# Optimization experiments

Measured on AMD Instinct MI355X. Metric: run time of the kernel, lower is better.

## Reference

```python
import jax, jax.numpy as jnp
import numpy as np

NH = 4       # n_heads
R = 3        # n_rounds
LN_EPS = 1e-5
NEG = -1e9   # large negative for masked attention (avoids NaN on fully-masked rows)


def _mha(q, k, v, w, b, block=None):
    # w: [4, D, D] = (Wq, Wk, Wv, Wo); b: [4, D]. batch_first MHA, no dropout (eval).
    B, Nq, Dm = q.shape
    hd = Dm // NH

    def proj(x, wi, bi):
        return (x @ wi + bi).reshape(B, -1, NH, hd).transpose(0, 2, 1, 3)  # [B,h,N,hd]

    Q = proj(q, w[0], b[0])
    K = proj(k, w[1], b[1])
    V = proj(v, w[2], b[2])
    s = jnp.einsum('bhqd,bhkd->bhqk', Q, K) * (1.0 / np.sqrt(hd))
    if block is not None:  # block[b,q,k]=True means masked out
        s = jnp.where(block[:, None, :, :], NEG, s)
    p = jax.nn.softmax(s, axis=-1)
    o = jnp.einsum('bhqk,bhkd->bhqd', p, V).transpose(0, 2, 1, 3).reshape(B, -1, Dm)
    return o @ w[3] + b[3]


def setup_inputs() -> dict:
    key = jax.random.key(0)
    ks = jax.random.split(key, 16)
    B, N, Dm = 256, 128, 256
    s = 0.02
    return {
        'H': jax.random.normal(ks[0], (B, N, Dm), jnp.float32),
        'pred_heads': jax.random.randint(ks[1], (B, N), 0, N),
        'mask': jnp.ones((B, N), jnp.float32),
        'ha_w': jax.random.normal(ks[2], (R, 4, Dm, Dm)) * s,
        'ha_b': jnp.zeros((R, 4, Dm)),
        'sa_w': jax.random.normal(ks[3], (R, 4, Dm, Dm)) * s,
        'sa_b': jnp.zeros((R, 4, Dm)),
        'ct_w': jax.random.normal(ks[4], (R, 2 * Dm, Dm)) * s,
        'ct_b': jnp.zeros((R, Dm)),
        'gate_w': jax.random.normal(ks[5], (R, 4 * Dm, Dm)) * s,
        'gate_b': jnp.zeros((R, Dm)),
        'tr_w': jax.random.normal(ks[6], (R, 4 * Dm, Dm)) * s,
        'tr_b': jnp.zeros((R, Dm)),
        'ln_g': jnp.ones((R, Dm)),
        'ln_b': jnp.zeros((R, Dm)),
        'arc_head_w': jax.random.normal(ks[7], (Dm, Dm)) * s,
        'arc_head_b': jnp.zeros((Dm,)),
        'arc_dep_w': jax.random.normal(ks[8], (Dm, Dm)) * s,
        'arc_dep_b': jnp.zeros((Dm,)),
        'bilinear': jax.random.normal(ks[9], (Dm, Dm)) * np.sqrt(2.0 / Dm).astype(np.float32),
        'bh_w': jax.random.normal(ks[10], (Dm,)) * s,
        'bh_b': jnp.zeros(()),
        'bd_w': jax.random.normal(ks[11], (Dm,)) * s,
        'bd_b': jnp.zeros(()),
    }


def reference(H, pred_heads, mask, ha_w, ha_b, sa_w, sa_b, ct_w, ct_b,
              gate_w, gate_b, tr_w, tr_b, ln_g, ln_b,
              arc_head_w, arc_head_b, arc_dep_w, arc_dep_b, bilinear,
              bh_w, bh_b, bd_w, bd_b):
    B, N, Dm = H.shape
    mb = mask > 0
    hi = jnp.clip(pred_heads, 0, N - 1)
    hi3 = jnp.broadcast_to(hi[:, :, None], (B, N, Dm))
    bidx = jnp.arange(B)[:, None]
    eye = jnp.eye(N, dtype=bool)
    # sibling mask: same predicted head, not self, both positions valid (constant across rounds)
    sib = (pred_heads[:, :, None] == pred_heads[:, None, :]) & ~eye[None] \
          & mb[:, None, :] & mb[:, :, None]
    block = ~sib

    Hr = H
    for i in range(R):
        # gather head representation, attend to it
        head_repr = jnp.take_along_axis(Hr, hi3, axis=1)
        head_msg = _mha(Hr, head_repr, head_repr, ha_w[i], ha_b[i])
        # scatter-add children onto their heads, average
        child_sum = jnp.zeros_like(Hr).at[bidx, hi].add(Hr)
        child_count = jnp.zeros((B, N), Hr.dtype).at[bidx, hi].add(mask)
        child_avg = child_sum / jnp.maximum(child_count, 1.0)[:, :, None]
        child_msg = jax.nn.gelu(
            jnp.concatenate([Hr, child_avg], -1) @ ct_w[i] + ct_b[i], approximate=False)
        # masked sibling self-attention (N <= 128 branch)
        sib_msg = _mha(Hr, Hr, Hr, sa_w[i], sa_b[i], block=block)
        # gated fuse + residual + LayerNorm
        comb = jnp.concatenate([Hr, head_msg, child_msg, sib_msg], -1)
        g = jax.nn.sigmoid(comb @ gate_w[i] + gate_b[i])
        u = jax.nn.gelu(comb @ tr_w[i] + tr_b[i], approximate=False)
        Hn = Hr + g * u
        mu = Hn.mean(-1, keepdims=True)
        var = ((Hn - mu) ** 2).mean(-1, keepdims=True)
        Hr = (Hn - mu) / jnp.sqrt(var + LN_EPS) * ln_g[i] + ln_b[i]

    h_head = Hr @ arc_head_w + arc_head_b
    h_dep = Hr @ arc_dep_w + arc_dep_b
    scores = jnp.einsum('bnd,de,bme->bnm', h_head, bilinear, h_dep)
    scores = scores + (h_head @ bh_w + bh_b)[:, None, :] + (h_dep @ bd_w + bd_b)[:, :, None]
    return Hr, scores
```

## Files before the change

### kernel.cpp

```cpp
#include <hip/hip_runtime.h>
#include <hip/hip_bf16.h>
#include <math.h>

typedef __hip_bfloat16 bf16;
typedef __attribute__((ext_vector_type(8))) short bf16x8v;
typedef __attribute__((ext_vector_type(4))) float f32x4v;

#define BD 256
#define NN 128
#define DM 256
#define NHD 4
#define HDIM 64
#define RR 3

__device__ __forceinline__ float b2f(bf16 x) { return __bfloat162float(x); }
__device__ __forceinline__ bf16 f2b(float x) { return __float2bfloat16(x); }
__device__ __forceinline__ float geluf(float x) { return 0.5f * x * (1.f + erff(x * 0.70710678118654752f)); }

#define GLOAD16(g, l) __builtin_amdgcn_global_load_lds( \
    (const __attribute__((address_space(1))) void*)(g), \
    (__attribute__((address_space(3))) void*)(l), 16, 0, 0)

__global__ __launch_bounds__(256) void cvt32to16_kernel(
    const float* __restrict__ in, bf16* __restrict__ out, int n)
{
  int i = blockIdx.x * 256 + threadIdx.x;
  int stride = gridDim.x * 256;
  for (; i < n; i += stride) out[i] = f2b(in[i]);
}

__global__ __launch_bounds__(256) void cvt16to32_kernel(
    const bf16* __restrict__ in, float* __restrict__ out, int n)
{
  int i = blockIdx.x * 256 + threadIdx.x;
  int stride = gridDim.x * 256;
  for (; i < n; i += stride) out[i] = b2f(in[i]);
}

struct TDesc { const float* src; bf16* dst; int K; int base; };
struct TTable { TDesc e[12]; };

__global__ __launch_bounds__(256) void transpose_w_kernel(TTable T, int nent)
{
  int t = blockIdx.x;
  int ei = 0;
  for (int i = 1; i < nent; i++) if (t >= T.e[i].base) ei = i;
  const float* src = T.e[ei].src;
  bf16* dst = T.e[ei].dst;
  int K = T.e[ei].K;
  int lt = t - T.e[ei].base;
  int nt = lt & 7, kt = lt >> 3;

  __shared__ float tile[32][33];
  int tx = threadIdx.x & 31, ty = threadIdx.x >> 5;
#pragma unroll
  for (int i = 0; i < 4; i++)
    tile[ty + i * 8][tx] = src[(size_t)(kt * 32 + ty + i * 8) * 256 + nt * 32 + tx];
  __syncthreads();
#pragma unroll
  for (int i = 0; i < 4; i++)
    dst[(size_t)(nt * 32 + ty + i * 8) * K + kt * 32 + tx] = f2b(tile[tx][ty + i * 8]);
}

struct FJob { const float* A; const float* B; bf16* outT; int koff; int kst; };
struct FJobs { FJob j[13]; };

__global__ __launch_bounds__(256) void wfuse_kernel(FJobs F)
{
  const FJob jb = F.j[blockIdx.y];
  const int k0 = blockIdx.x * 16;
  const int col = threadIdx.x;
  float acc[16];
#pragma unroll
  for (int i = 0; i < 16; i++) acc[i] = 0.f;
  for (int m = 0; m < 256; m++) {
    float bv = jb.B[(size_t)m * 256 + col];
#pragma unroll
    for (int i = 0; i < 16; i++)
      acc[i] += jb.A[(size_t)(k0 + i) * 256 + m] * bv;
  }
#pragma unroll
  for (int i = 0; i < 16; i++)
    jb.outT[(size_t)col * jb.kst + jb.koff + k0 + i] = f2b(acc[i]);
}

__global__ __launch_bounds__(256) void bfuse_kernel(
    const float* gate_w, const float* tr_w, const float* gate_b, const float* tr_b,
    const float* ha_b, const float* sa_b,
    const float* ahw, const float* ahb, const float* bil,
    const float* bhw, const float* bhb,
    float* fgb, float* ftb, float* fab_bias, float* vha, float* cha)
{
  int blk = blockIdx.x, col = threadIdx.x;
  if (blk < 6) {
    int r = blk >> 1; bool isT = blk & 1;
    const float* W  = (isT ? tr_w : gate_w) + (size_t)r * 262144;
    const float* b0 = (isT ? tr_b : gate_b) + (size_t)r * 256;
    const float* boh = ha_b + (size_t)r * 1024 + 768;
    const float* bos = sa_b + (size_t)r * 1024 + 768;
    float acc = b0[col];
    for (int m = 0; m < 256; m++) {
      acc += boh[m] * W[(size_t)(256 + m) * 256 + col];
      acc += bos[m] * W[(size_t)(768 + m) * 256 + col];
    }
    ((isT ? ftb : fgb) + (size_t)r * 256)[col] = acc;
  } else {
    float a1 = 0.f, a2 = 0.f;
    for (int m = 0; m < 256; m++) {
      a1 += ahb[m] * bil[(size_t)m * 256 + col];
      a2 += ahw[(size_t)col * 256 + m] * bhw[m];
    }
    fab_bias[col] = a1;
    vha[col] = a2;
    if (col == 0) {
      float c = bhb[0];
      for (int m = 0; m < 256; m++) c += ahb[m] * bhw[m];
      cha[0] = c;
    }
  }
}

struct ProjArgs {
  const bf16* Hc; const bf16* CA; const int* gather;
  const bf16* W[7];
  const float* bias[7];
  bf16* out[7];
};

__global__ __launch_bounds__(256) void proj_fused_kernel(ProjArgs P)
{
  const int b  = blockIdx.x & 255;
  const int nh = blockIdx.x >> 8;
  const int c0 = nh * 128;
  const int tid = threadIdx.x;
  const int w = tid >> 6;
  const int lane = tid & 63;
  const int wr = w >> 1, wc = w & 1;
  const int r16 = lane & 15;
  const int kg = lane >> 4;

  __shared__ __align__(16) char lds[81920];

  const char* Hb = (const char*)(P.Hc + (size_t)b * NN * DM);

#pragma unroll
  for (int i = 0; i < 16; i++) {
    int row = w * 32 + i * 2 + (lane >> 5);
    int src = row * 512 + (((lane & 31) * 16) ^ ((row & 7) << 4));
    GLOAD16(Hb + src, lds + w * 16384 + i * 1024);
  }

#define STAGE_W(WT, K2, KT, BUF) do { \
    _Pragma("unroll") \
    for (int i_ = 0; i_ < 2; i_++) { \
      int wrow_ = w * 32 + i_ * 16 + (lane >> 2); \
      int slot_ = (lane & 3) ^ ((wrow_ >> 1) & 3); \
      GLOAD16((const char*)(WT) + (size_t)(c0 + wrow_) * (K2) + (KT) * 64 + slot_ * 16, \
              lds + 65536 + (BUF) * 8192 + w * 2048 + i_ * 1024); \
    } } while (0)

  STAGE_W(P.W[0], 512, 0, 0);
  __syncthreads();

  int lrow[4], grow[4];
#pragma unroll
  for (int mi = 0; mi < 4; mi++) {
    lrow[mi] = wr * 64 + mi * 16 + r16;
    int g = P.gather[b * NN + lrow[mi]];
    grow[mi] = min(max(g, 0), NN - 1);
  }
  int wro[4];
#pragma unroll
  for (int ni = 0; ni < 4; ni++) {
    int ct_ = wc * 64 + ni * 16 + r16;
    wro[ni] = ct_ * 64 + ((kg ^ ((ct_ >> 1) & 3)) << 4);
  }

  const bf16* CAb = P.CA + (size_t)b * NN * DM;
  int buf = 0;
  f32x4v zero = {0.f, 0.f, 0.f, 0.f};

#pragma unroll
  for (int j = 0; j < 7; j++) {
    const bool GATH = (j == 1) || (j == 2);
    const bool TR   = (j == 2) || (j == 5);
    const bool ACT  = (j == 6);
    const int NKS = (j == 6) ? 16 : 8;
    const int K2  = (j == 6) ? 1024 : 512;
    const bf16* Wj  = P.W[j];
    const bf16* Wj1 = (j < 6) ? P.W[j + 1] : P.W[j];
    const int  K2n  = (j < 6) ? ((j + 1 == 6) ? 1024 : 512) : K2;

    f32x4v acc[4][4];
#pragma unroll
    for (int mi = 0; mi < 4; mi++)
#pragma unroll
      for (int ni = 0; ni < 4; ni++) acc[mi][ni] = zero;

    for (int kt = 0; kt < NKS; kt++) {
      if (!(j == 6 && kt + 1 == NKS)) {
        const bf16* Wn = (kt + 1 < NKS) ? Wj : Wj1;
        int nkt = (kt + 1 < NKS) ? kt + 1 : 0;
        int nK2 = (kt + 1 < NKS) ? K2 : K2n;
        STAGE_W(Wn, nK2, nkt, buf ^ 1);
      }

      bf16x8v a[4], wv[4];
      if (j == 6 && kt >= 8) {
#pragma unroll
        for (int mi = 0; mi < 4; mi++)
          a[mi] = *(const bf16x8v*)(CAb + (size_t)lrow[mi] * DM + (kt - 8) * 32 + kg * 8);
      } else {
#pragma unroll
        for (int mi = 0; mi < 4; mi++) {
          int ar = GATH ? grow[mi] : lrow[mi];
          int off = ar * 512 + (((kt * 64) + kg * 16) ^ ((ar & 7) << 4));
          a[mi] = *(const bf16x8v*)(lds + off);
        }
      }
#pragma unroll
      for (int ni = 0; ni < 4; ni++)
        wv[ni] = *(const bf16x8v*)(lds + 65536 + buf * 8192 + wro[ni]);

#pragma unroll
      for (int mi = 0; mi < 4; mi++)
#pragma unroll
        for (int ni = 0; ni < 4; ni++)
          acc[mi][ni] = __builtin_amdgcn_mfma_f32_16x16x32_bf16(a[mi], wv[ni], acc[mi][ni], 0, 0, 0);

      __syncthreads();
      buf ^= 1;
    }

    bf16* outj = P.out[j];
    const float* bj = P.bias[j];
#pragma unroll
    for (int ni = 0; ni < 4; ni++) {
      int col = c0 + wc * 64 + ni * 16 + r16;
      float bv = bj ? bj[col] : 0.f;
#pragma unroll
      for (int mi = 0; mi < 4; mi++) {
        int row0 = wr * 64 + mi * 16 + kg * 4;
        if (!TR) {
          size_t base = ((size_t)b * NN + row0) * DM + col;
#pragma unroll
          for (int r = 0; r < 4; r++) {
            float x = acc[mi][ni][r] + bv;
            if (ACT) x = geluf(x);
            outj[base + (size_t)r * DM] = f2b(x);
          }
        } else {
          size_t base = ((size_t)b * DM + col) * NN + row0;
#pragma unroll
          for (int r = 0; r < 4; r++)
            outj[base + r] = f2b(acc[mi][ni][r] + bv);
        }
      }
    }
  }
#undef STAGE_W
}

struct GJob {
  const bf16 *a0, *a1, *a2, *a3;
  const int* gather;
  const bf16* Wt;
  const float* bias;
  bf16* out;
  int K, act, transp;
};
struct GJobs8 { GJob j[8]; };

__global__ __launch_bounds__(256) void gemm_multi_kernel(GJobs8 J)
{
  const GJob jb = J.j[blockIdx.y];
  const int b  = blockIdx.x & 255;
  const int nh = blockIdx.x >> 8;
  const int tid = threadIdx.x;
  const int w = tid >> 6;
  const int lane = tid & 63;
  const int wr = w >> 1, wc = w & 1;
  const int r16 = lane & 15;
  const int kg = lane >> 4;
  const int K = jb.K;
  const int nk = K >> 5;
  const int c0 = nh * 128;

  __shared__ __align__(16) char lds[32768];

  const int srow = tid >> 2;
  const int skc  = tid & 3;
  const int sl   = skc ^ ((srow >> 1) & 3);
  int g0 = srow, g1 = srow + 64;
  if (jb.gather) {
    int t0 = jb.gather[b * NN + srow];      g0 = min(max(t0, 0), NN - 1);
    int t1 = jb.gather[b * NN + srow + 64]; g1 = min(max(t1, 0), NN - 1);
  }
  const size_t aoff0 = ((size_t)b * NN + g0) * DM + sl * 8;
  const size_t aoff1 = ((size_t)b * NN + g1) * DM + sl * 8;
  const bf16* wsrc0 = jb.Wt + (size_t)(c0 + srow) * K + sl * 8;
  const bf16* wsrc1 = jb.Wt + (size_t)(c0 + srow + 64) * K + sl * 8;
  const int wbase = w * 1024;

  f32x4v zero = {0.f, 0.f, 0.f, 0.f};
  f32x4v acc[4][4];
#pragma unroll
  for (int mi = 0; mi < 4; mi++)
#pragma unroll
    for (int ni = 0; ni < 4; ni++) acc[mi][ni] = zero;

  int a_ro[4], w_ro[4];
#pragma unroll
  for (int mi = 0; mi < 4; mi++) {
    int row = wr * 64 + mi * 16 + r16;
    a_ro[mi] = row * 64 + ((kg ^ ((row >> 1) & 3)) << 4);
  }
#pragma unroll
  for (int ni = 0; ni < 4; ni++) {
    int col = wc * 64 + ni * 16 + r16;
    w_ro[ni] = col * 64 + ((kg ^ ((col >> 1) & 3)) << 4);
  }

  {
    const bf16* Ab = jb.a0;
    GLOAD16(Ab + aoff0, lds + wbase);
    GLOAD16(Ab + aoff1, lds + 4096 + wbase);
    GLOAD16(wsrc0,      lds + 16384 + wbase);
    GLOAD16(wsrc1,      lds + 16384 + 4096 + wbase);
  }
  __syncthreads();

  int cur = 0;
  for (int kt = 0; kt < nk; kt++) {
    if (kt + 1 < nk) {
      int k0 = (kt + 1) << 5;
      int sg = k0 >> 8;
      const bf16* Ab = (sg == 0) ? jb.a0 : ((sg == 1) ? jb.a1 : ((sg == 2) ? jb.a2 : jb.a3));
      int ko = k0 & 255;
      int nb = (cur ^ 1) * 8192;
      GLOAD16(Ab + aoff0 + ko,  lds + nb + wbase);
      GLOAD16(Ab + aoff1 + ko,  lds + nb + 4096 + wbase);
      GLOAD16(wsrc0 + k0,       lds + 16384 + nb + wbase);
      GLOAD16(wsrc1 + k0,       lds + 16384 + nb + 4096 + wbase);
    }

    const char* La = lds + cur * 8192;
    const char* Lw = lds + 16384 + cur * 8192;
    bf16x8v a[4], ww[4];
#pragma unroll
    for (int mi = 0; mi < 4; mi++) a[mi] = *(const bf16x8v*)(La + a_ro[mi]);
#pragma unroll
    for (int ni = 0; ni < 4; ni++) ww[ni] = *(const bf16x8v*)(Lw + w_ro[ni]);
#pragma unroll
    for (int mi = 0; mi < 4; mi++)
#pragma unroll
      for (int ni = 0; ni < 4; ni++)
        acc[mi][ni] = __builtin_amdgcn_mfma_f32_16x16x32_bf16(a[mi], ww[ni], acc[mi][ni], 0, 0, 0);

    __syncthreads();
    cur ^= 1;
  }

#pragma unroll
  for (int ni = 0; ni < 4; ni++) {
    int col = c0 + wc * 64 + ni * 16 + r16;
    float bv = jb.bias ? jb.bias[col] : 0.f;
#pragma unroll
    for (int mi = 0; mi < 4; mi++) {
      int row0 = wr * 64 + mi * 16 + kg * 4;
      if (!jb.transp) {
        size_t base = ((size_t)b * NN + row0) * DM + col;
#pragma unroll
        for (int r = 0; r < 4; r++) {
          float x = acc[mi][ni][r] + bv;
          if (jb.act == 1) x = geluf(x);
          jb.out[base + (size_t)r * DM] = f2b(x);
        }
      } else {
        size_t base = ((size_t)b * DM + col) * NN + row0;
#pragma unroll
        for (int r = 0; r < 4; r++) {
          float x = acc[mi][ni][r] + bv;
          if (jb.act == 1) x = geluf(x);
          jb.out[base + r] = f2b(x);
        }
      }
    }
  }
}

struct AttnArgs {
  const bf16 *Qa, *Ka, *Va; bf16* Oa;
  const bf16 *Qs, *Ks, *Vs; bf16* Os;
};

__global__ __launch_bounds__(256) void attn2_kernel(
    AttnArgs A, const int* __restrict__ ph, const float* __restrict__ mask)
{
  const int b = blockIdx.y, h = blockIdx.x;
  const bool has_mask = (blockIdx.z == 1);
  const bf16* Qb = has_mask ? A.Qs : A.Qa;
  const bf16* Kb = has_mask ? A.Ks : A.Ka;
  const bf16* Vt = has_mask ? A.Vs : A.Va;
  bf16* Ob       = has_mask ? A.Os : A.Oa;

  const int w = threadIdx.x >> 6;
  const int lane = threadIdx.x & 63;
  const int r16 = lane & 15, kg = lane >> 4;
  const int q0 = w * 32;

  __shared__ bf16 P_lds[4][32 * 128];
  __shared__ int   ph_sh[NN];
  __shared__ float mk_sh[NN];

  if (has_mask && threadIdx.x < NN) {
    ph_sh[threadIdx.x] = ph[(size_t)b * NN + threadIdx.x];
    mk_sh[threadIdx.x] = mask[(size_t)b * NN + threadIdx.x];
  }
  __syncthreads();

  const bf16* Qh = Qb + (size_t)b * NN * DM + (size_t)h * HDIM;
  const bf16* Kh = Kb + (size_t)b * NN * DM + (size_t)h * HDIM;
  const bf16* Vh = Vt + ((size_t)b * DM + (size_t)h * HDIM) * NN;

  f32x4v zero = {0.f, 0.f, 0.f, 0.f};

  f32x4v accs[2][8];
#pragma unroll
  for (int mi = 0; mi < 2; mi++)
#pragma unroll
    for (int ni = 0; ni < 8; ni++) accs[mi][ni] = zero;

#pragma unroll
  for (int ks = 0; ks < 2; ks++) {
    int d = ks * 32 + kg * 8;
    bf16x8v a[2], bb[8];
#pragma unroll
    for (int mi = 0; mi < 2; mi++)
      a[mi] = *(const bf16x8v*)(Qh + (size_t)(q0 + mi * 16 + r16) * DM + d);
#pragma unroll
    for (int ni = 0; ni < 8; ni++)
      bb[ni] = *(const bf16x8v*)(Kh + (size_t)(ni * 16 + r16) * DM + d);
#pragma unroll
    for (int mi = 0; mi < 2; mi++)
#pragma unroll
      for (int ni = 0; ni < 8; ni++)
        accs[mi][ni] = __builtin_amdgcn_mfma_f32_16x16x32_bf16(a[mi], bb[ni], accs[mi][ni], 0, 0, 0);
  }

#pragma unroll
  for (int mi = 0; mi < 2; mi++) {
#pragma unroll
    for (int r = 0; r < 4; r++) {
      int wq = mi * 16 + kg * 4 + r;
      int q_e = q0 + wq;
      float v[8];
      float mx = -3.0e38f;
      int qp = 0; float qm = 1.f;
      if (has_mask) { qp = ph_sh[q_e]; qm = mk_sh[q_e]; }
#pragma unroll
      for (int ni = 0; ni < 8; ni++) {
        float s = accs[mi][ni][r] * 0.125f;
        if (has_mask) {
          int t_e = ni * 16 + r16;
          bool sib = (qp == ph_sh[t_e]) && (q_e != t_e) && (qm > 0.f) && (mk_sh[t_e] > 0.f);
          if (!sib) s = -1e9f;
        }
        v[ni] = s;
        mx = fmaxf(mx, s);
      }
#pragma unroll
      for (int o = 1; o < 16; o <<= 1) mx = fmaxf(mx, __shfl_xor(mx, o, 64));
      float sum = 0.f;
#pragma unroll
      for (int ni = 0; ni < 8; ni++) { v[ni] = __expf(v[ni] - mx); sum += v[ni]; }
#pragma unroll
      for (int o = 1; o < 16; o <<= 1) sum += __shfl_xor(sum, o, 64);
      float inv = 1.f / sum;
      int swz = (wq & 7) << 3;
#pragma unroll
      for (int ni = 0; ni < 8; ni++) {
        int t_e = ni * 16 + r16;
        P_lds[w][(wq * 128 + t_e) ^ swz] = f2b(v[ni] * inv);
      }
    }
  }
  __syncthreads();

  f32x4v acco[2][4];
#pragma unroll
  for (int mi = 0; mi < 2; mi++)
#pragma unroll
    for (int ni = 0; ni < 4; ni++) acco[mi][ni] = zero;

#pragma unroll
  for (int kt = 0; kt < 4; kt++) {
    int t = kt * 32 + kg * 8;
    bf16x8v a[2], bb[4];
#pragma unroll
    for (int mi = 0; mi < 2; mi++) {
      int wqr = mi * 16 + r16;
      int idx = (wqr * 128 + t) ^ ((wqr & 7) << 3);
      a[mi] = *(const bf16x8v*)&P_lds[w][idx];
    }
#pragma unroll
    for (int ni = 0; ni < 4; ni++)
      bb[ni] = *(const bf16x8v*)(Vh + (size_t)(ni * 16 + r16) * NN + t);
#pragma unroll
    for (int mi = 0; mi < 2; mi++)
#pragma unroll
      for (int ni = 0; ni < 4; ni++)
        acco[mi][ni] = __builtin_amdgcn_mfma_f32_16x16x32_bf16(a[mi], bb[ni], acco[mi][ni], 0, 0, 0);
  }

#pragma unroll
  for (int ni = 0; ni < 4; ni++) {
    int d = ni * 16 + r16;
#pragma unroll
    for (int mi = 0; mi < 2; mi++) {
      int qrow = q0 + mi * 16 + kg * 4;
      size_t base = ((size_t)b * NN + qrow) * DM + (size_t)h * HDIM + d;
#pragma unroll
      for (int r = 0; r < 4; r++)
        Ob[base + (size_t)r * DM] = f2b(acco[mi][ni][r]);
    }
  }
}

__global__ __launch_bounds__(256) void child_avg2_kernel(
    const bf16* __restrict__ Hr, const int* __restrict__ ph,
    const float* __restrict__ mask, bf16* __restrict__ CA)
{
  const int b = blockIdx.x;
  const int t = threadIdx.x;
  __shared__ int hi[NN];
  __shared__ float mk[NN];
  __shared__ int cnt[NN], off[NN], rnk[NN], lst[NN];
  __shared__ float cntf[NN];

  if (t < NN) {
    int g = ph[(size_t)b * NN + t];
    hi[t] = min(max(g, 0), NN - 1);
    mk[t] = mask[(size_t)b * NN + t];
  }
  __syncthreads();
  if (t < NN) {
    int c = 0, r = 0; float cf = 0.f;
    int me = hi[t];
    for (int j = 0; j < NN; j++) {
      int hj = hi[j];
      c  += (hj == t);
      cf += (hj == t) ? mk[j] : 0.f;
      r  += (j < t) && (hj == me);
    }
    cnt[t] = c; cntf[t] = cf; rnk[t] = r;
  }
  __syncthreads();
  if (t < NN) {
    int o = 0;
    for (int m = 0; m < t; m++) o += cnt[m];
    off[t] = o;
  }
  __syncthreads();
  if (t < NN) lst[off[hi[t]] + rnk[t]] = t;
  __syncthreads();

  const bf16* Hb = Hr + (size_t)b * NN * DM;
  bf16* Cb = CA + (size_t)b * NN * DM;
  const int d = t;
  for (int m = 0; m < NN; m++) {
    float s = 0.f;
    int o = off[m], c = cnt[m];
    for (int i = 0; i < c; i++)
      s += b2f(Hb[(size_t)lst[o + i] * DM + d]);
    Cb[(size_t)m * DM + d] = f2b(s / fmaxf(cntf[m], 1.f));
  }
}

__global__ __launch_bounds__(256) void ln_epi_kernel(
    const bf16* __restrict__ Hr, const bf16* __restrict__ Gp, const bf16* __restrict__ Up,
    const float* __restrict__ lg, const float* __restrict__ lb, bf16* __restrict__ Hout)
{
  const int b = blockIdx.y;
  const int m0 = blockIdx.x * 8;
  const int c = threadIdx.x;
  __shared__ float red[8];
  float lgv = lg[c], lbv = lb[c];
  int wv = c >> 6, ln = c & 63;
  for (int m = 0; m < 8; m++) {
    size_t idx = ((size_t)b * NN + m0 + m) * DM + c;
    float g = 1.f / (1.f + __expf(-b2f(Gp[idx])));
    float u = geluf(b2f(Up[idx]));
    float hn = b2f(Hr[idx]) + g * u;
    float s1 = hn, s2 = hn * hn;
#pragma unroll
    for (int o = 1; o < 64; o <<= 1) { s1 += __shfl_xor(s1, o, 64); s2 += __shfl_xor(s2, o, 64); }
    if (ln == 0) { red[wv] = s1; red[4 + wv] = s2; }
    __syncthreads();
    float sum = red[0] + red[1] + red[2] + red[3];
    float sq  = red[4] + red[5] + red[6] + red[7];
    float mu = sum * (1.f / DM);
    float var = sq * (1.f / DM) - mu * mu;
    float y = (hn - mu) * rsqrtf(var + 1e-5f) * lgv + lbv;
    Hout[idx] = f2b(y);
    __syncthreads();
  }
}

__global__ __launch_bounds__(256) void rhrd2_kernel(
    const bf16* __restrict__ Hc, const bf16* __restrict__ hd,
    const float* __restrict__ vha, const float* __restrict__ cha,
    const float* __restrict__ bdw, const float* __restrict__ bdb,
    float* __restrict__ rh, float* __restrict__ rd)
{
  int b = blockIdx.x;
  int t = threadIdx.x;
  int n = t & 127;
  bool isD = t >= 128;
  if (!isD) {
    const bf16* row = Hc + ((size_t)b * NN + n) * DM;
    float s = cha[0];
    for (int k = 0; k < DM; k++) s += b2f(row[k]) * vha[k];
    rh[(size_t)b * NN + n] = s;
  } else {
    const bf16* row = hd + ((size_t)b * NN + n) * DM;
    float s = bdb[0];
    for (int k = 0; k < DM; k++) s += b2f(row[k]) * bdw[k];
    rd[(size_t)b * NN + n] = s;
  }
}

__global__ __launch_bounds__(512) void scores_mfma_kernel(
    const bf16* __restrict__ tmp, const bf16* __restrict__ hd,
    const float* __restrict__ rh, const float* __restrict__ rd,
    float* __restrict__ out)
{
  const int b = blockIdx.x;
  const int w = threadIdx.x >> 6;
  const int lane = threadIdx.x & 63;
  const int wr = w >> 1, wc = w & 1;
  const int r16 = lane & 15;
  const int kg = lane >> 4;

  size_t qoff[2], moff[4];
#pragma unroll
  for (int mi = 0; mi < 2; mi++) qoff[mi] = ((size_t)b * NN + wr * 32 + mi * 16 + r16) * DM;
#pragma unroll
  for (int ni = 0; ni < 4; ni++) moff[ni] = ((size_t)b * NN + wc * 64 + ni * 16 + r16) * DM;

  f32x4v zero = {0.f, 0.f, 0.f, 0.f};
  f32x4v acc[2][4];
#pragma unroll
  for (int mi = 0; mi < 2; mi++)
#pragma unroll
    for (int ni = 0; ni < 4; ni++) acc[mi][ni] = zero;

  for (int k0 = 0; k0 < DM; k0 += 32) {
    int k = k0 + kg * 8;
    bf16x8v a[2], bb[4];
#pragma unroll
    for (int mi = 0; mi < 2; mi++) a[mi] = *(const bf16x8v*)(tmp + qoff[mi] + k);
#pragma unroll
    for (int ni = 0; ni < 4; ni++) bb[ni] = *(const bf16x8v*)(hd + moff[ni] + k);
#pragma unroll
    for (int mi = 0; mi < 2; mi++)
#pragma unroll
      for (int ni = 0; ni < 4; ni++)
        acc[mi][ni] = __builtin_amdgcn_mfma_f32_16x16x32_bf16(a[mi], bb[ni], acc[mi][ni], 0, 0, 0);
  }

#pragma unroll
  for (int ni = 0; ni < 4; ni++) {
    int m = wc * 64 + ni * 16 + r16;
    float rhm = rh[b * NN + m];
#pragma unroll
    for (int mi = 0; mi < 2; mi++) {
      int q0 = wr * 32 + mi * 16 + kg * 4;
#pragma unroll
      for (int r = 0; r < 4; r++)
        out[(size_t)b * NN * NN + (size_t)(q0 + r) * NN + m] =
            acc[mi][ni][r] + rhm + rd[b * NN + q0 + r];
    }
  }
}

extern "C" void kernel_launch(void* const* d_in, const int* in_sizes, int n_in,
                              void* d_out, int out_size, void* d_ws, size_t ws_size,
                              hipStream_t stream) {
  const float* H      = (const float*)d_in[0];
  const int*   ph     = (const int*)  d_in[1];
  const float* mask   = (const float*)d_in[2];
  const float* ha_w   = (const float*)d_in[3];
  const float* ha_b   = (const float*)d_in[4];
  const float* sa_w   = (const float*)d_in[5];
  const float* sa_b   = (const float*)d_in[6];
  const float* ct_w   = (const float*)d_in[7];
  const float* ct_b   = (const float*)d_in[8];
  const float* gate_w = (const float*)d_in[9];
  const float* gate_b = (const float*)d_in[10];
  const float* tr_w   = (const float*)d_in[11];
  const float* tr_b   = (const float*)d_in[12];
  const float* ln_g   = (const float*)d_in[13];
  const float* ln_b   = (const float*)d_in[14];
  const float* ahw    = (const float*)d_in[15];
  const float* ahb    = (const float*)d_in[16];
  const float* adw    = (const float*)d_in[17];
  const float* adb    = (const float*)d_in[18];
  const float* bil    = (const float*)d_in[19];
  const float* bhw    = (const float*)d_in[20];
  const float* bhb    = (const float*)d_in[21];
  const float* bdw    = (const float*)d_in[22];
  const float* bdb    = (const float*)d_in[23];

  const size_t AB = (size_t)BD * NN * DM;
  bf16* wsb  = (bf16*)d_ws;
  bf16* Hcur = wsb + 0 * AB;
  bf16* Qa   = wsb + 1 * AB;
  bf16* Ka   = wsb + 2 * AB;
  bf16* Va   = wsb + 3 * AB;
  bf16* Qs   = wsb + 4 * AB;
  bf16* Ks   = wsb + 5 * AB;
  bf16* Vs   = wsb + 6 * AB;
  bf16* mC   = wsb + 7 * AB;
  float* rh  = (float*)(wsb + 8 * AB);
  float* rd  = rh + (size_t)BD * NN;
  float* fgb = rd + (size_t)BD * NN;
  float* ftb = fgb + 768;
  float* fab_bias = ftb + 768;
  float* vha = fab_bias + 256;
  float* cha = vha + 256;

  bf16* D0 = (bf16*)d_out;
  bf16* D1 = D0 + AB;
  bf16* D2 = D0 + 2 * AB;
  const size_t RS = 1179648;
  bf16* adT  = D2 + 3 * RS;
  bf16* fabT = adT + 65536;

  cvt32to16_kernel<<<dim3(2048), 256, 0, stream>>>(H, Hcur, (int)AB);

  for (int r = 0; r < RR; r++) {
    bf16* base_r = D2 + (size_t)r * RS;
    bf16* haT = base_r;
    bf16* saT = base_r + 262144;
    bf16* ctT = base_r + 524288;
    bf16* gT  = base_r + 655360;
    bf16* tT  = base_r + 917504;
    TTable T; int base = 0;
    for (int i = 0; i < 3; i++) {
      T.e[i] = { ha_w + ((size_t)r * 4 + i) * 65536, haT + (size_t)i * 65536, 256, base };
      base += 64;
    }
    for (int i = 0; i < 3; i++) {
      T.e[3 + i] = { sa_w + ((size_t)r * 4 + i) * 65536, saT + (size_t)i * 65536, 256, base };
      base += 64;
    }
    T.e[6] = { ct_w + (size_t)r * 131072, ctT, 512, base };                    base += 128;
    T.e[7] = { gate_w + (size_t)r * 262144,             gT,        1024, base }; base += 64;
    T.e[8] = { gate_w + (size_t)r * 262144 + 512 * 256, gT + 512,  1024, base }; base += 64;
    T.e[9] = { tr_w   + (size_t)r * 262144,             tT,        1024, base }; base += 64;
    T.e[10]= { tr_w   + (size_t)r * 262144 + 512 * 256, tT + 512,  1024, base }; base += 64;
    int nent = 11;
    if (r == 0) { T.e[11] = { adw, adT, 256, base }; base += 64; nent = 12; }
    transpose_w_kernel<<<dim3(base), 256, 0, stream>>>(T, nent);
  }
  {
    FJobs F;
    for (int r = 0; r < RR; r++) {
      bf16* gT = D2 + (size_t)r * RS + 655360;
      bf16* tT = D2 + (size_t)r * RS + 917504;
      const float* WoH = ha_w + ((size_t)r * 4 + 3) * 65536;
      const float* WoS = sa_w + ((size_t)r * 4 + 3) * 65536;
      const float* gw = gate_w + (size_t)r * 262144;
      const float* tw = tr_w   + (size_t)r * 262144;
      F.j[r * 4 + 0] = { WoH, gw + 256 * 256, gT, 256, 1024 };
      F.j[r * 4 + 1] = { WoS, gw + 768 * 256, gT, 768, 1024 };
      F.j[r * 4 + 2] = { WoH, tw + 256 * 256, tT, 256, 1024 };
      F.j[r * 4 + 3] = { WoS, tw + 768 * 256, tT, 768, 1024 };
    }
    F.j[12] = { ahw, bil, fabT, 0, 256 };
    wfuse_kernel<<<dim3(16, 13), 256, 0, stream>>>(F);
  }
  bfuse_kernel<<<dim3(7), 256, 0, stream>>>(gate_w, tr_w, gate_b, tr_b,
      ha_b, sa_b, ahw, ahb, bil, bhw, bhb, fgb, ftb, fab_bias, vha, cha);

  for (int r = 0; r < RR; r++) {
    bf16* base_r = D2 + (size_t)r * RS;
    bf16* haT = base_r;
    bf16* saT = base_r + 262144;
    bf16* ctT = base_r + 524288;
    bf16* gT  = base_r + 655360;
    bf16* tT  = base_r + 917504;
    const float* hab = ha_b + (size_t)r * 4 * DM;
    const float* sab = sa_b + (size_t)r * 4 * DM;

    child_avg2_kernel<<<dim3(BD), 256, 0, stream>>>(Hcur, ph, mask, D0);

    {
      ProjArgs P;
      P.Hc = Hcur; P.CA = D0; P.gather = ph;
      P.W[0] = haT;          P.bias[0] = hab + 0;   P.out[0] = Qa;
      P.W[1] = haT + 65536;  P.bias[1] = hab + 256; P.out[1] = Ka;
      P.W[2] = haT + 131072; P.bias[2] = hab + 512; P.out[2] = Va;
      P.W[3] = saT;          P.bias[3] = sab + 0;   P.out[3] = Qs;
      P.W[4] = saT + 65536;  P.bias[4] = sab + 256; P.out[4] = Ks;
      P.W[5] = saT + 131072; P.bias[5] = sab + 512; P.out[5] = Vs;
      P.W[6] = ctT;          P.bias[6] = ct_b + (size_t)r * DM; P.out[6] = mC;
      proj_fused_kernel<<<dim3(512), 256, 0, stream>>>(P);
    }

    {
      AttnArgs A = { Qa, Ka, Va, D0, Qs, Ks, Vs, D1 };
      attn2_kernel<<<dim3(NHD, BD, 2), 256, 0, stream>>>(A, ph, mask);
    }

    {
      GJobs8 J = {};
      J.j[0] = { Hcur, D0, mC, D1, nullptr, gT, fgb + (size_t)r * 256, Va, 1024, 0, 0 };
      J.j[1] = { Hcur, D0, mC, D1, nullptr, tT, ftb + (size_t)r * 256, Vs, 1024, 0, 0 };
      gemm_multi_kernel<<<dim3(512, 2), 256, 0, stream>>>(J);
    }

    ln_epi_kernel<<<dim3(16, BD), 256, 0, stream>>>(Hcur, Va, Vs,
        ln_g + (size_t)r * DM, ln_b + (size_t)r * DM, Hcur);
  }

  {
    GJobs8 J = {};
    J.j[0] = { Hcur, Hcur, Hcur, Hcur, nullptr, adT,  adb,      Ka, 256, 0, 0 };
    J.j[1] = { Hcur, Hcur, Hcur, Hcur, nullptr, fabT, fab_bias, Va, 256, 0, 0 };
    gemm_multi_kernel<<<dim3(512, 2), 256, 0, stream>>>(J);
  }
  rhrd2_kernel<<<dim3(BD), 256, 0, stream>>>(Hcur, Ka, vha, cha, bdw, bdb, rh, rd);
  scores_mfma_kernel<<<dim3(BD), 512, 0, stream>>>(Va, Ka, rh, rd, (float*)d_out + AB);

  cvt16to32_kernel<<<dim3(2048), 256, 0, stream>>>(Hcur, (float*)d_out, (int)AB);
}
```

Measured before the change: 1.012 ms.

## Share A tile across gate and transform GEMMs in one 512-thread block

Replaces the two-job multi-GEMM launch with a dual-weight kernel in which each 512-thread block loads the activation tile once and computes both output GEMMs (gate and transform, or arc-dep and fused head), with half the waves assigned to each weight matrix. This halves the global reads of the shared A operand and the number of blocks. In exchange each block uses more LDS (48KB) and threads, which can lower occupancy, and the unused gather/transpose/activation paths are dropped.

Measured after the change: 936.4 us, median of 2. 1.08x faster.

```diff
diff --git a/kernel.cpp b/kernel.cpp
--- a/kernel.cpp
+++ b/kernel.cpp
@@ -261,45 +261,38 @@
 #undef STAGE_W
 }
 
-struct GJob {
+struct DJob {
   const bf16 *a0, *a1, *a2, *a3;
-  const int* gather;
-  const bf16* Wt;
-  const float* bias;
-  bf16* out;
-  int K, act, transp;
+  const bf16 *W0, *W1;
+  const float *b0, *b1;
+  bf16 *o0, *o1;
+  int K;
 };
-struct GJobs8 { GJob j[8]; };
-
-__global__ __launch_bounds__(256) void gemm_multi_kernel(GJobs8 J)
-{
-  const GJob jb = J.j[blockIdx.y];
+
+__global__ __launch_bounds__(512) void dualw_gemm_kernel(DJob jb)
+{
   const int b  = blockIdx.x & 255;
   const int nh = blockIdx.x >> 8;
+  const int c0 = nh * 128;
   const int tid = threadIdx.x;
   const int w = tid >> 6;
+  const int jj = w >> 2;
+  const int wsub = w & 3;
+  const int wr = wsub >> 1, wc = wsub & 1;
   const int lane = tid & 63;
-  const int wr = w >> 1, wc = w & 1;
   const int r16 = lane & 15;
   const int kg = lane >> 4;
   const int K = jb.K;
   const int nk = K >> 5;
-  const int c0 = nh * 128;
-
-  __shared__ __align__(16) char lds[32768];
+
+  __shared__ __align__(16) char lds[49152];
 
   const int srow = tid >> 2;
   const int skc  = tid & 3;
   const int sl   = skc ^ ((srow >> 1) & 3);
-  int g0 = srow, g1 = srow + 64;
-  if (jb.gather) {
-    int t0 = jb.gather[b * NN + srow];      g0 = min(max(t0, 0), NN - 1);
-    int t1 = jb.gather[b * NN + srow + 64]; g1 = min(max(t1, 0), NN - 1);
-  }
-  const size_t aoff0 = ((size_t)b * NN + g0) * DM + sl * 8;
-  const size_t aoff1 = ((size_t)b * NN + g1) * DM + sl * 8;
-  const bf16* wsrc0 = jb.Wt + (size_t)(c0 + srow) * K + sl * 8;
-  const bf16* wsrc1 = jb.Wt + (size_t)(c0 + srow + 64) * K + sl * 8;
+  const size_t aoff = ((size_t)b * NN + srow) * DM + sl * 8;
+  const bf16* w0src = jb.W0 + (size_t)(c0 + srow) * K + sl * 8;
+  const bf16* w1src = jb.W1 + (size_t)(c0 + srow) * K + sl * 8;
   const int wbase = w * 1024;
 
   f32x4v zero = {0.f, 0.f, 0.f, 0.f};
@@ -315,6 +308,7 @@
     int row = wr * 64 + mi * 16 + r16;
     a_ro[mi] = row * 64 + ((kg ^ ((row >> 1) & 3)) << 4);
   }
+  const int wsel = 16384 + jj * 16384;
 #pragma unroll
   for (int ni = 0; ni < 4; ni++) {
     int col = wc * 64 + ni * 16 + r16;
@@ -322,11 +316,9 @@
   }
 
   {
-    const bf16* Ab = jb.a0;
-    GLOAD16(Ab + aoff0, lds + wbase);
-    GLOAD16(Ab + aoff1, lds + 4096 + wbase);
-    GLOAD16(wsrc0,      lds + 16384 + wbase);
-    GLOAD16(wsrc1,      lds + 16384 + 4096 + wbase);
+    GLOAD16(jb.a0 + aoff, lds + wbase);
+    GLOAD16(w0src,        lds + 16384 + wbase);
+    GLOAD16(w1src,        lds + 32768 + wbase);
   }
   __syncthreads();
 
@@ -338,14 +330,13 @@
       const bf16* Ab = (sg == 0) ? jb.a0 : ((sg == 1) ? jb.a1 : ((sg == 2) ? jb.a2 : jb.a3));
       int ko = k0 & 255;
       int nb = (cur ^ 1) * 8192;
-      GLOAD16(Ab + aoff0 + ko,  lds + nb + wbase);
-      GLOAD16(Ab + aoff1 + ko,  lds + nb + 4096 + wbase);
-      GLOAD16(wsrc0 + k0,       lds + 16384 + nb + wbase);
-      GLOAD16(wsrc1 + k0,       lds + 16384 + nb + 4096 + wbase);
+      GLOAD16(Ab + aoff + ko,  lds + nb + wbase);
+      GLOAD16(w0src + k0,      lds + 16384 + nb + wbase);
+      GLOAD16(w1src + k0,      lds + 32768 + nb + wbase);
     }
 
     const char* La = lds + cur * 8192;
-    const char* Lw = lds + 16384 + cur * 8192;
+    const char* Lw = lds + wsel + cur * 8192;
     bf16x8v a[4], ww[4];
 #pragma unroll
     for (int mi = 0; mi < 4; mi++) a[mi] = *(const bf16x8v*)(La + a_ro[mi]);
@@ -361,30 +352,19 @@
     cur ^= 1;
   }
 
+  bf16* out = jj ? jb.o1 : jb.o0;
+  const float* bias = jj ? jb.b1 : jb.b0;
 #pragma unroll
   for (int ni = 0; ni < 4; ni++) {
     int col = c0 + wc * 64 + ni * 16 + r16;
-    float bv = jb.bias ? jb.bias[col] : 0.f;
+    float bv = bias ? bias[col] : 0.f;
 #pragma unroll
     for (int mi = 0; mi < 4; mi++) {
       int row0 = wr * 64 + mi * 16 + kg * 4;
-      if (!jb.transp) {
-        size_t base = ((size_t)b * NN + row0) * DM + col;
-#pragma unroll
-        for (int r = 0; r < 4; r++) {
-          float x = acc[mi][ni][r] + bv;
-          if (jb.act == 1) x = geluf(x);
-          jb.out[base + (size_t)r * DM] = f2b(x);
-        }
-      } else {
-        size_t base = ((size_t)b * DM + col) * NN + row0;
-#pragma unroll
-        for (int r = 0; r < 4; r++) {
-          float x = acc[mi][ni][r] + bv;
-          if (jb.act == 1) x = geluf(x);
-          jb.out[base + r] = f2b(x);
-        }
-      }
+      size_t base = ((size_t)b * NN + row0) * DM + col;
+#pragma unroll
+      for (int r = 0; r < 4; r++)
+        out[base + (size_t)r * DM] = f2b(acc[mi][ni][r] + bv);
     }
   }
 }
@@ -815,10 +795,9 @@
     }
 
     {
-      GJobs8 J = {};
-      J.j[0] = { Hcur, D0, mC, D1, nullptr, gT, fgb + (size_t)r * 256, Va, 1024, 0, 0 };
-      J.j[1] = { Hcur, D0, mC, D1, nullptr, tT, ftb + (size_t)r * 256, Vs, 1024, 0, 0 };
-      gemm_multi_kernel<<<dim3(512, 2), 256, 0, stream>>>(J);
+      DJob J = { Hcur, D0, mC, D1, gT, tT,
+                 fgb + (size_t)r * 256, ftb + (size_t)r * 256, Va, Vs, 1024 };
+      dualw_gemm_kernel<<<dim3(512), 512, 0, stream>>>(J);
     }
 
     ln_epi_kernel<<<dim3(16, BD), 256, 0, stream>>>(Hcur, Va, Vs,
@@ -826,10 +805,8 @@
   }
 
   {
-    GJobs8 J = {};
-    J.j[0] = { Hcur, Hcur, Hcur, Hcur, nullptr, adT,  adb,      Ka, 256, 0, 0 };
-    J.j[1] = { Hcur, Hcur, Hcur, Hcur, nullptr, fabT, fab_bias, Va, 256, 0, 0 };
-    gemm_multi_kernel<<<dim3(512, 2), 256, 0, stream>>>(J);
+    DJob J = { Hcur, Hcur, Hcur, Hcur, adT, fabT, adb, fab_bias, Ka, Va, 256 };
+    dualw_gemm_kernel<<<dim3(512), 512, 0, stream>>>(J);
   }
   rhrd2_kernel<<<dim3(BD), 256, 0, stream>>>(Hcur, Ka, vha, cha, bdw, bdb, rh, rd);
   scores_mfma_kernel<<<dim3(BD), 512, 0, stream>>>(Va, Ka, rh, rd, (float*)d_out + AB);
```
